# Optimization experiments

Measured on AMD Instinct MI355X. Metric: run time of the kernel, lower is better.

The kernel has to match this reference:

```python
import jax, jax.numpy as jnp
import numpy as np

N, E = 50000, 640000
IN, HD, OUT, NCLS = 768, 128, 128, 2
H, C = 4, 32  # heads, per-head channels (HD/H = OUT/H = 32)
NEG_SLOPE = 0.2


def _glorot(key, shape):
    fan_in, fan_out = shape[0], shape[1]
    lim = jnp.sqrt(6.0 / (fan_in + fan_out))
    return jax.random.uniform(key, shape, jnp.float32, -lim, lim)


def setup_inputs() -> dict:
    key = jax.random.key(0)
    ks = jax.random.split(key, 24)
    x = jax.random.normal(ks[0], (1, N, IN), jnp.float32)
    edge_index = jax.random.randint(ks[1], (2, E), 0, N, jnp.int64)
    d = {"x": x, "edge_index": edge_index}
    ins = [IN, HD, HD, HD]
    for i in range(4):
        d[f"Wl{i+1}"] = _glorot(ks[2 + 5 * i], (ins[i], H * C))
        d[f"Wr{i+1}"] = _glorot(ks[3 + 5 * i], (ins[i], H * C))
        d[f"att{i+1}"] = _glorot(ks[4 + 5 * i], (H, C))
        d[f"b{i+1}"] = jnp.zeros((H * C,), jnp.float32)
    d["clfW"] = _glorot(ks[22], (OUT, NCLS))
    d["clfb"] = jnp.zeros((NCLS,), jnp.float32)
    return d


def _gatv2_layer(x, Wl, Wr, att, b, src, dst):
    # x: [N, F_in] -> out: [N, H*C]. GATv2: e = a^T LeakyReLU(xl_j + xr_i)
    xl = (x @ Wl).reshape(N, H, C)
    xr = (x @ Wr).reshape(N, H, C)
    h = xl[src] + xr[dst]                                   # [E', H, C] per-edge gather
    e = jnp.einsum('ehc,hc->eh', jax.nn.leaky_relu(h, NEG_SLOPE), att)
    m = jax.ops.segment_max(e, dst, num_segments=N)          # scatter-softmax (stable)
    a = jnp.exp(e - m[dst])
    s = jax.ops.segment_sum(a, dst, num_segments=N)
    alpha = a / (s[dst] + 1e-16)
    out = jax.ops.segment_sum(alpha[..., None] * xl[src], dst, num_segments=N)
    return out.reshape(N, H * C) + b


def reference(x, edge_index, Wl1, Wr1, att1, b1, Wl2, Wr2, att2, b2,
              Wl3, Wr3, att3, b3, Wl4, Wr4, att4, b4, clfW, clfb):
    xn = x.reshape(N, IN)  # torch.squeeze
    loops = jnp.arange(N, dtype=edge_index.dtype)  # PyG add_self_loops=True
    src = jnp.concatenate([edge_index[0], loops])
    dst = jnp.concatenate([edge_index[1], loops])
    h = jax.nn.relu(_gatv2_layer(xn, Wl1, Wr1, att1, b1, src, dst))
    h = jax.nn.relu(_gatv2_layer(h, Wl2, Wr2, att2, b2, src, dst))
    h = jax.nn.relu(_gatv2_layer(h, Wl3, Wr3, att3, b3, src, dst))
    h = _gatv2_layer(h, Wl4, Wr4, att4, b4, src, dst)        # [N, OUT]
    g = jnp.mean(h, axis=0, keepdims=True)                   # unsqueeze+mean over nodes -> [1, OUT]
    return g @ clfW + clfb                                   # [1, NCLS]
```

## Files before the change

kernel.cpp:

```cpp
#include <hip/hip_runtime.h>
#include <hip/hip_bf16.h>
#include <hip/hip_fp16.h>

#define NN 50000
#define EE 640000
#define HC 128
#define NB1 196
#define NEB 6250

typedef _Float16 f16x8 __attribute__((ext_vector_type(8)));
typedef _Float16 h2 __attribute__((ext_vector_type(2)));
typedef float f32x4 __attribute__((ext_vector_type(4)));
typedef unsigned short u16;

__device__ __forceinline__ u16 f2h(float f) {
    return __builtin_bit_cast(u16, (_Float16)f);
}
__device__ __forceinline__ h2 bch2(unsigned a) { return __builtin_bit_cast(h2, a); }
__device__ __forceinline__ h2 habs2(h2 a) {
    return __builtin_bit_cast(h2, __builtin_bit_cast(unsigned, a) & 0x7FFF7FFFu);
}

__device__ __forceinline__ void gload_lds16(const void* g, void* l) {
    __builtin_amdgcn_global_load_lds((const __attribute__((address_space(1))) void*)g,
                                     (__attribute__((address_space(3))) void*)l, 16, 0, 0);
}

__device__ __forceinline__ float red8(float x) {
    x += __int_as_float(__builtin_amdgcn_update_dpp(0, __float_as_int(x), 0xB1, 0xF, 0xF, true));
    x += __int_as_float(__builtin_amdgcn_update_dpp(0, __float_as_int(x), 0x4E, 0xF, 0xF, true));
    x += __int_as_float(__builtin_amdgcn_ds_swizzle(__float_as_int(x), 0x101F));
    return x;
}


__global__ void k_count(const int* __restrict__ ei, int* __restrict__ cnt) {
    int e = blockIdx.x * blockDim.x + threadIdx.x;
    if (e < EE) atomicAdd(&cnt[ei[EE + e]], 1);
}

__global__ void k_bsum(const int* __restrict__ cnt, int* __restrict__ bsum) {
    __shared__ int sd[256];
    int b = blockIdx.x, t = threadIdx.x, i = b * 256 + t;
    sd[t] = (i < NN) ? cnt[i] + 1 : 0;
    __syncthreads();
    for (int o = 128; o; o >>= 1) { if (t < o) sd[t] += sd[t + o]; __syncthreads(); }
    if (!t) bsum[b] = sd[0];
}

__global__ void k_offs(const int* __restrict__ cnt_in, const int* __restrict__ bsum,
                       int* __restrict__ offs, int* __restrict__ cursor,
                       int* __restrict__ csr) {
    __shared__ int sb[256];
    __shared__ int sd[256];
    int b = blockIdx.x, t = threadIdx.x, i = b * 256 + t;
    sb[t] = (t < NB1) ? bsum[t] : 0;
    int v = (i < NN) ? cnt_in[i] + 1 : 0;
    sd[t] = v;
    __syncthreads();
    for (int o = 1; o < 256; o <<= 1) {
        int u1 = (t >= o) ? sd[t - o] : 0;
        int u2 = (t >= o) ? sb[t - o] : 0;
        __syncthreads();
        sd[t] += u1; sb[t] += u2;
        __syncthreads();
    }
    int bex = (b > 0) ? sb[b - 1] : 0;
    if (i < NN) {
        int o = bex + sd[t] - v;
        offs[i] = o;
        csr[o] = i;
        cursor[i] = o + 1;
    }
    if (b == NB1 - 1 && t == 0) offs[NN] = sb[NB1 - 1];
}

__global__ void k_fill(const int* __restrict__ ei, int* __restrict__ cursor,
                       int* __restrict__ csr) {
    int e = blockIdx.x * blockDim.x + threadIdx.x;
    if (e < EE) {
        int s = ei[e], d = ei[EE + e];
        int pos = atomicAdd(&cursor[d], 1);
        csr[pos] = s;
    }
}


#define WT_L0 196608
#define WT_LX 32768
#define WT_TOT (WT_L0 + 3 * WT_LX)

__global__ void k_castw_all(const float* __restrict__ Wl1, const float* __restrict__ Wr1,
                            const float* __restrict__ Wl2, const float* __restrict__ Wr2,
                            const float* __restrict__ Wl3, const float* __restrict__ Wr3,
                            const float* __restrict__ Wl4, const float* __restrict__ Wr4,
                            u16* __restrict__ WtAll) {
    int gid = blockIdx.x * 256 + threadIdx.x;
    if (gid >= WT_TOT) return;
    const float *Wl, *Wr;
    int idx, K, base;
    if (gid < WT_L0) { Wl = Wl1; Wr = Wr1; idx = gid; K = 768; base = 0; }
    else {
        int r = gid - WT_L0;
        int l = r >> 15; idx = r & (WT_LX - 1); K = 128; base = WT_L0 + l * WT_LX;
        if (l == 0)      { Wl = Wl2; Wr = Wr2; }
        else if (l == 1) { Wl = Wl3; Wr = Wr3; }
        else             { Wl = Wl4; Wr = Wr4; }
    }
    int c = idx / K, k = idx - c * K;
    float v = (c < 128) ? Wl[k * 128 + c] : Wr[k * 128 + (c - 128)];
    WtAll[base + idx] = f2h(v);
}


__global__ __launch_bounds__(512, 4)
void k_gemm0(const float* __restrict__ Af, const u16* __restrict__ Wt,
             u16* __restrict__ xb) {
    constexpr int K = 768;
    __shared__ __align__(16) u16 As[128 * 64];
    __shared__ __align__(16) u16 Bs[256 * 64];
    const int tid = threadIdx.x;
    const int wv = tid >> 6, ln = tid & 63;
    const int wr = wv >> 2, wc = wv & 3;
    const int m0 = blockIdx.x * 128;
    const int lrow = ln & 15, g = ln >> 4;

    f32x4 acc[4][4] = {};

    const int arow = tid >> 2, aq = tid & 3;
    int arg = m0 + arow; if (arg >= NN) arg = 0;
    float4 ra0, ra1, ra2, ra3;

    {
        const float* src = Af + (size_t)arg * K + aq * 16;
        ra0 = *(const float4*)(src);
        ra1 = *(const float4*)(src + 4);
        ra2 = *(const float4*)(src + 8);
        ra3 = *(const float4*)(src + 12);
    }

    constexpr int NSTEP = K / 64;
    for (int ks = 0; ks < NSTEP; ++ks) {
        {
            const int s = arow & 7;
            f16x8 v0, v1;
            v0[0] = (_Float16)ra0.x; v0[1] = (_Float16)ra0.y;
            v0[2] = (_Float16)ra0.z; v0[3] = (_Float16)ra0.w;
            v0[4] = (_Float16)ra1.x; v0[5] = (_Float16)ra1.y;
            v0[6] = (_Float16)ra1.z; v0[7] = (_Float16)ra1.w;
            v1[0] = (_Float16)ra2.x; v1[1] = (_Float16)ra2.y;
            v1[2] = (_Float16)ra2.z; v1[3] = (_Float16)ra2.w;
            v1[4] = (_Float16)ra3.x; v1[5] = (_Float16)ra3.y;
            v1[6] = (_Float16)ra3.z; v1[7] = (_Float16)ra3.w;
            *(f16x8*)&As[arow * 64 + (((aq * 2) ^ s) * 8)] = v0;
            *(f16x8*)&As[arow * 64 + (((aq * 2 + 1) ^ s) * 8)] = v1;
        }
        #pragma unroll
        for (int q = 0; q < 4; ++q) {
            int r8 = (wv * 4 + q) * 8;
            int row = r8 + (ln >> 3);
            int lc = (ln & 7) ^ (row & 7);
            gload_lds16(Wt + (size_t)row * K + ks * 64 + lc * 8, &Bs[r8 * 64]);
        }
        __syncthreads();

        if (ks + 1 < NSTEP) {
            const float* src = Af + (size_t)arg * K + (ks + 1) * 64 + aq * 16;
            ra0 = *(const float4*)(src);
            ra1 = *(const float4*)(src + 4);
            ra2 = *(const float4*)(src + 8);
            ra3 = *(const float4*)(src + 12);
        }

        #pragma unroll
        for (int kk = 0; kk < 2; ++kk) {
            f16x8 af[4], bfr[4];
            #pragma unroll
            for (int f = 0; f < 4; ++f) {
                int r = wr * 64 + f * 16 + lrow;
                af[f] = *(const f16x8*)&As[r * 64 + (((kk * 4 + g) ^ (r & 7)) * 8)];
                int c = wc * 64 + f * 16 + lrow;
                bfr[f] = *(const f16x8*)&Bs[c * 64 + (((kk * 4 + g) ^ (c & 7)) * 8)];
            }
            #pragma unroll
            for (int i = 0; i < 4; ++i)
                #pragma unroll
                for (int j = 0; j < 4; ++j)
                    acc[i][j] = __builtin_amdgcn_mfma_f32_16x16x32_f16(af[i], bfr[j], acc[i][j], 0, 0, 0);
        }
        __syncthreads();
    }

    const int crow0 = m0 + wr * 64 + (g << 2);
    const int ccol0 = wc * 64 + lrow;
    #pragma unroll
    for (int i = 0; i < 4; ++i)
        #pragma unroll
        for (int rr = 0; rr < 4; ++rr) {
            int row = crow0 + i * 16 + rr;
            if (row < NN) {
                #pragma unroll
                for (int j = 0; j < 4; ++j)
                    xb[(size_t)row * 256 + ccol0 + j * 16] = f2h(acc[i][j][rr]);
            }
        }
}


__global__ __launch_bounds__(512)
void k_gemm_s(const u16* __restrict__ A, const u16* __restrict__ Wt,
              u16* __restrict__ xb) {
    __shared__ __align__(16) u16 As[128 * 128];
    const int tid = threadIdx.x;
    const int wv = tid >> 6, ln = tid & 63;
    const int wr = wv >> 2, wc = wv & 3;
    const int m0 = blockIdx.x * 128;
    const int lrow = ln & 15, g = ln >> 4;

    #pragma unroll
    for (int q = 0; q < 4; ++q) {
        int seg = wv * 4 + q;
        int row = seg * 4 + g;
        int lc = lrow ^ (row & 15);
        int rg = m0 + row; if (rg >= NN) rg = 0;
        gload_lds16(A + (size_t)rg * 128 + lc * 8, &As[seg * 512]);
    }
    f16x8 bfr[4][4];
    #pragma unroll
    for (int j = 0; j < 4; ++j) {
        int col = wc * 64 + j * 16 + lrow;
        #pragma unroll
        for (int kk = 0; kk < 4; ++kk)
            bfr[j][kk] = *(const f16x8*)&Wt[(size_t)col * 128 + kk * 32 + g * 8];
    }
    __syncthreads();

    f32x4 acc[4][4] = {};
    #pragma unroll
    for (int kk = 0; kk < 4; ++kk) {
        f16x8 af[4];
        #pragma unroll
        for (int f = 0; f < 4; ++f) {
            int r = wr * 64 + f * 16 + lrow;
            int pc = (kk * 4 + g) ^ (r & 15);
            af[f] = *(const f16x8*)&As[r * 128 + pc * 8];
        }
        #pragma unroll
        for (int i = 0; i < 4; ++i)
            #pragma unroll
            for (int j = 0; j < 4; ++j)
                acc[i][j] = __builtin_amdgcn_mfma_f32_16x16x32_f16(af[i], bfr[j][kk], acc[i][j], 0, 0, 0);
    }

    const int crow0 = m0 + wr * 64 + (g << 2);
    const int ccol0 = wc * 64 + lrow;
    #pragma unroll
    for (int i = 0; i < 4; ++i)
        #pragma unroll
        for (int rr = 0; rr < 4; ++rr) {
            int row = crow0 + i * 16 + rr;
            if (row < NN) {
                #pragma unroll
                for (int j = 0; j < 4; ++j)
                    xb[(size_t)row * 256 + ccol0 + j * 16] = f2h(acc[i][j][rr]);
            }
        }
}


__global__ __launch_bounds__(256)
void k_edge(const u16* __restrict__ xb, const float* __restrict__ att,
            const float* __restrict__ bias, const int* __restrict__ offs,
            const int* __restrict__ csr, u16* __restrict__ outb,
            float* __restrict__ part, int relu) {
    __shared__ float ps[HC];
    const int wv = threadIdx.x >> 6;
    const int ln = threadIdx.x & 63;
    const int half = ln >> 5, lh = ln & 31;
    const int i = blockIdx.x * 8 + wv * 2 + half;
    const int c4 = lh * 4;

    if (part && threadIdx.x < HC) ps[threadIdx.x] = 0.f;

    uint2 xrw = *(const uint2*)&xb[(size_t)i * 256 + 128 + c4];
    const h2 xr01 = bch2(xrw.x), xr23 = bch2(xrw.y);
    float4 av = *(const float4*)&att[c4];
    const h2 at01 = {(_Float16)av.x, (_Float16)av.y};
    const h2 at23 = {(_Float16)av.z, (_Float16)av.w};
    const h2 C06 = {(_Float16)0.6f, (_Float16)0.6f};
    const h2 C04 = {(_Float16)0.4f, (_Float16)0.4f};

    int beg = offs[i];
    int deg = offs[i + 1] - beg;
    int degO = __shfl_xor(deg, 32);
    int degM = (deg > degO) ? deg : degO;

    float m0v = -3.0e38f, s0v = 0.f, a00 = 0.f, a01 = 0.f, a02 = 0.f, a03 = 0.f;
    float m1v = -3.0e38f, s1v = 0.f, a10 = 0.f, a11 = 0.f, a12 = 0.f, a13 = 0.f;
    float m2v = -3.0e38f, s2v = 0.f, a20 = 0.f, a21 = 0.f, a22 = 0.f, a23 = 0.f;
    float m3v = -3.0e38f, s3v = 0.f, a30 = 0.f, a31 = 0.f, a32 = 0.f, a33 = 0.f;

#define GATH(k, jj) uint2 w##k = *(const uint2*)&xb[(size_t)(jj) * 256 + c4];
#define UPD(k, M, S, A0, A1, A2, A3, ok) { \
    h2 v01 = bch2(w##k.x), v23 = bch2(w##k.y); \
    h2 u01 = v01 + xr01, u23 = v23 + xr23; \
    h2 l01 = u01 * C06 + habs2(u01) * C04; \
    h2 l23 = u23 * C06 + habs2(u23) * C04; \
    float e = __builtin_amdgcn_fdot2(l01, at01, \
              __builtin_amdgcn_fdot2(l23, at23, 0.f, false), false); \
    e = red8(e); \
    float d = e - M; \
    float tt = __expf(-fabsf(d)); \
    bool ng = (d <= 0.f) || (!(ok)); \
    float c = ng ? 1.f : tt; \
    float ww = (ok) ? (ng ? tt : 1.f) : 0.f; \
    M = ng ? M : e; \
    S = S * c + ww; \
    A0 = A0 * c + ww * (float)v01[0]; A1 = A1 * c + ww * (float)v01[1]; \
    A2 = A2 * c + ww * (float)v23[0]; A3 = A3 * c + ww * (float)v23[1]; }

    for (int base = 0; base < degM; base += 32) {
        int idxv = (base + lh < deg) ? csr[beg + base + lh] : i;
        int lim = degM - base; if (lim > 32) lim = 32;
        int myl = deg - base;
        for (int p = 0; p < lim; p += 4) {
            int j0 = __shfl(idxv, p + 0, 32);
            int j1 = __shfl(idxv, p + 1, 32);
            int j2 = __shfl(idxv, p + 2, 32);
            int j3 = __shfl(idxv, p + 3, 32);
            GATH(0, j0) GATH(1, j1) GATH(2, j2) GATH(3, j3)
            UPD(0, m0v, s0v, a00, a01, a02, a03, (p + 0 < myl))
            UPD(1, m1v, s1v, a10, a11, a12, a13, (p + 1 < myl))
            UPD(2, m2v, s2v, a20, a21, a22, a23, (p + 2 < myl))
            UPD(3, m3v, s3v, a30, a31, a32, a33, (p + 3 < myl))
        }
    }
#undef GATH
#undef UPD

    float mm = fmaxf(fmaxf(m0v, m1v), fmaxf(m2v, m3v));
    float c0 = __expf(m0v - mm), c1 = __expf(m1v - mm);
    float c2 = __expf(m2v - mm), c3 = __expf(m3v - mm);
    float s = s0v * c0 + s1v * c1 + s2v * c2 + s3v * c3 + 1e-16f;
    float inv = 1.f / s;
    float4 bv = *(const float4*)&bias[c4];
    float o0 = (a00 * c0 + a10 * c1 + a20 * c2 + a30 * c3) * inv + bv.x;
    float o1 = (a01 * c0 + a11 * c1 + a21 * c2 + a31 * c3) * inv + bv.y;
    float o2 = (a02 * c0 + a12 * c1 + a22 * c2 + a32 * c3) * inv + bv.z;
    float o3 = (a03 * c0 + a13 * c1 + a23 * c2 + a33 * c3) * inv + bv.w;
    if (relu) {
        o0 = fmaxf(o0, 0.f); o1 = fmaxf(o1, 0.f);
        o2 = fmaxf(o2, 0.f); o3 = fmaxf(o3, 0.f);
    }
    if (outb) {
        uint2 pk;
        pk.x = (unsigned)f2h(o0) | ((unsigned)f2h(o1) << 16);
        pk.y = (unsigned)f2h(o2) | ((unsigned)f2h(o3) << 16);
        *(uint2*)&outb[(size_t)i * HC + c4] = pk;
    }
    if (part) {
        __syncthreads();
        atomicAdd(&ps[c4 + 0], o0);
        atomicAdd(&ps[c4 + 1], o1);
        atomicAdd(&ps[c4 + 2], o2);
        atomicAdd(&ps[c4 + 3], o3);
        __syncthreads();
        if (threadIdx.x < HC)
            part[(size_t)blockIdx.x * HC + threadIdx.x] = ps[threadIdx.x];
    }
}


__global__ __launch_bounds__(256)
void k_colsum(const float* __restrict__ h, float* __restrict__ gsum, int nr) {
    __shared__ float4 sd[8][32];
    int t = threadIdx.x;
    int c4 = t & 31, rl = t >> 5;
    float sx = 0.f, sy = 0.f, sz = 0.f, sw = 0.f;
    for (int r = blockIdx.x * 8 + rl; r < nr; r += 8 * gridDim.x) {
        float4 v = *(const float4*)&h[(size_t)r * HC + c4 * 4];
        sx += v.x; sy += v.y; sz += v.z; sw += v.w;
    }
    sd[rl][c4] = make_float4(sx, sy, sz, sw);
    __syncthreads();
    if (rl == 0) {
        float4 a = sd[0][c4];
        #pragma unroll
        for (int q = 1; q < 8; ++q) {
            float4 b = sd[q][c4];
            a.x += b.x; a.y += b.y; a.z += b.z; a.w += b.w;
        }
        atomicAdd(&gsum[c4 * 4 + 0], a.x);
        atomicAdd(&gsum[c4 * 4 + 1], a.y);
        atomicAdd(&gsum[c4 * 4 + 2], a.z);
        atomicAdd(&gsum[c4 * 4 + 3], a.w);
    }
}

__global__ void k_clf(const float* __restrict__ gsum, const float* __restrict__ W,
                      const float* __restrict__ bcls, float* __restrict__ out) {
    __shared__ float v[HC];
    int t = threadIdx.x;
    v[t] = gsum[t] * (1.f / (float)NN);
    __syncthreads();
    if (t < 2) {
        float r = 0.f;
        for (int k = 0; k < HC; ++k) r += v[k] * W[k * 2 + t];
        out[t] = r + bcls[t];
    }
}


extern "C" void kernel_launch(void* const* d_in, const int* in_sizes, int n_in,
                              void* d_out, int out_size, void* d_ws, size_t ws_size,
                              hipStream_t stream) {
    const float* x = (const float*)d_in[0];
    const int* ei = (const int*)d_in[1];
    const float *Wl[4], *Wr[4], *att[4], *bia[4];
    for (int l = 0; l < 4; ++l) {
        Wl[l] = (const float*)d_in[2 + 4 * l];
        Wr[l] = (const float*)d_in[3 + 4 * l];
        att[l] = (const float*)d_in[4 + 4 * l];
        bia[l] = (const float*)d_in[5 + 4 * l];
    }
    const float* clfW = (const float*)d_in[18];
    const float* clfb = (const float*)d_in[19];
    float* outp = (float*)d_out;

    char* w = (char*)d_ws;
    size_t o = 0;
    auto alloc = [&](size_t bytes) {
        char* p = w + o;
        o = (o + bytes + 255) & ~(size_t)255;
        return p;
    };
    int* cnt    = (int*)alloc((size_t)NN * 4);
    float* gsum = (float*)alloc(HC * 4);
    size_t zspan = o;
    int* offs  = (int*)alloc((size_t)(NN + 1) * 4);
    int* csr   = (int*)alloc((size_t)(EE + NN) * 4);
    int* bsum  = (int*)alloc((size_t)NB1 * 4);
    u16* WtAll = (u16*)alloc((size_t)WT_TOT * 2);
    u16* xb    = (u16*)alloc((size_t)NN * 256 * 2);
    u16* hb0   = (u16*)alloc((size_t)NN * HC * 2);
    u16* hb1   = (u16*)alloc((size_t)NN * HC * 2);
    float* part = (float*)alloc((size_t)NEB * HC * 4);

    hipMemsetAsync(cnt, 0, zspan, stream);
    k_count<<<(EE + 255) / 256, 256, 0, stream>>>(ei, cnt);
    k_bsum<<<NB1, 256, 0, stream>>>(cnt, bsum);
    k_offs<<<NB1, 256, 0, stream>>>(cnt, bsum, offs, cnt, csr);
    k_fill<<<(EE + 255) / 256, 256, 0, stream>>>(ei, cnt, csr);
    k_castw_all<<<(WT_TOT + 255) / 256, 256, 0, stream>>>(
        Wl[0], Wr[0], Wl[1], Wr[1], Wl[2], Wr[2], Wl[3], Wr[3], WtAll);

    const int GB = (NN + 127) / 128;
    const u16* Wt_l[4] = {WtAll, WtAll + WT_L0, WtAll + WT_L0 + WT_LX,
                          WtAll + WT_L0 + 2 * WT_LX};
    const u16* hb_in = nullptr;
    u16* hbb[2] = {hb0, hb1};
    for (int l = 0; l < 4; ++l) {
        if (l == 0) k_gemm0<<<GB, 512, 0, stream>>>(x, Wt_l[0], xb);
        else        k_gemm_s<<<GB, 512, 0, stream>>>(hb_in, Wt_l[l], xb);
        u16* ob = (l < 3) ? hbb[l & 1] : nullptr;
        float* pp = (l == 3) ? part : nullptr;
        k_edge<<<NEB, 256, 0, stream>>>(xb, att[l], bia[l], offs, csr, ob, pp,
                                        (l < 3) ? 1 : 0);
        hb_in = ob;
    }

    k_colsum<<<64, 256, 0, stream>>>(part, gsum, NEB);
    k_clf<<<1, 128, 0, stream>>>(gsum, clfW, clfb, outp);
}
```

Measured before the change: 372.0 us.

## Double-buffer GEMM weight loads, replace final-layer block partials with full output

In the shared-weight GEMM, B fragments are now loaded one k-slice ahead instead of all sixteen up front, which cuts register pressure and overlaps global loads with MFMAs. The final edge layer no longer reduces through shared-memory atomics and two block barriers. It writes the full fp32 per-node output, and a wider colsum grid reduces it. The reduction helper also swaps a ds_swizzle for a DPP row-rotate. The trade is an extra ~25MB fp32 write and read in exchange for removing the atomics and barriers.

```diff
diff --git a/kernel.cpp b/kernel.cpp
--- a/kernel.cpp
+++ b/kernel.cpp
@@ -29,7 +29,7 @@
 __device__ __forceinline__ float red8(float x) {
     x += __int_as_float(__builtin_amdgcn_update_dpp(0, __float_as_int(x), 0xB1, 0xF, 0xF, true));
     x += __int_as_float(__builtin_amdgcn_update_dpp(0, __float_as_int(x), 0x4E, 0xF, 0xF, true));
-    x += __int_as_float(__builtin_amdgcn_ds_swizzle(__float_as_int(x), 0x101F));
+    x += __int_as_float(__builtin_amdgcn_update_dpp(0, __float_as_int(x), 0x141, 0xF, 0xF, true));
     return x;
 }
 
@@ -225,19 +225,23 @@
         int rg = m0 + row; if (rg >= NN) rg = 0;
         gload_lds16(A + (size_t)rg * 128 + lc * 8, &As[seg * 512]);
     }
-    f16x8 bfr[4][4];
-    #pragma unroll
-    for (int j = 0; j < 4; ++j) {
-        int col = wc * 64 + j * 16 + lrow;
-        #pragma unroll
-        for (int kk = 0; kk < 4; ++kk)
-            bfr[j][kk] = *(const f16x8*)&Wt[(size_t)col * 128 + kk * 32 + g * 8];
-    }
+    const int bcol = wc * 64 + lrow;
+    f16x8 b0_ = *(const f16x8*)&Wt[(size_t)(bcol     ) * 128 + g * 8];
+    f16x8 b1_ = *(const f16x8*)&Wt[(size_t)(bcol + 16) * 128 + g * 8];
+    f16x8 b2_ = *(const f16x8*)&Wt[(size_t)(bcol + 32) * 128 + g * 8];
+    f16x8 b3_ = *(const f16x8*)&Wt[(size_t)(bcol + 48) * 128 + g * 8];
     __syncthreads();
 
     f32x4 acc[4][4] = {};
     #pragma unroll
     for (int kk = 0; kk < 4; ++kk) {
+        f16x8 n0_, n1_, n2_, n3_;
+        if (kk < 3) {
+            n0_ = *(const f16x8*)&Wt[(size_t)(bcol     ) * 128 + (kk + 1) * 32 + g * 8];
+            n1_ = *(const f16x8*)&Wt[(size_t)(bcol + 16) * 128 + (kk + 1) * 32 + g * 8];
+            n2_ = *(const f16x8*)&Wt[(size_t)(bcol + 32) * 128 + (kk + 1) * 32 + g * 8];
+            n3_ = *(const f16x8*)&Wt[(size_t)(bcol + 48) * 128 + (kk + 1) * 32 + g * 8];
+        }
         f16x8 af[4];
         #pragma unroll
         for (int f = 0; f < 4; ++f) {
@@ -246,10 +250,13 @@
             af[f] = *(const f16x8*)&As[r * 128 + pc * 8];
         }
         #pragma unroll
-        for (int i = 0; i < 4; ++i)
-            #pragma unroll
-            for (int j = 0; j < 4; ++j)
-                acc[i][j] = __builtin_amdgcn_mfma_f32_16x16x32_f16(af[i], bfr[j][kk], acc[i][j], 0, 0, 0);
+        for (int i = 0; i < 4; ++i) {
+            acc[i][0] = __builtin_amdgcn_mfma_f32_16x16x32_f16(af[i], b0_, acc[i][0], 0, 0, 0);
+            acc[i][1] = __builtin_amdgcn_mfma_f32_16x16x32_f16(af[i], b1_, acc[i][1], 0, 0, 0);
+            acc[i][2] = __builtin_amdgcn_mfma_f32_16x16x32_f16(af[i], b2_, acc[i][2], 0, 0, 0);
+            acc[i][3] = __builtin_amdgcn_mfma_f32_16x16x32_f16(af[i], b3_, acc[i][3], 0, 0, 0);
+        }
+        if (kk < 3) { b0_ = n0_; b1_ = n1_; b2_ = n2_; b3_ = n3_; }
     }
 
     const int crow0 = m0 + wr * 64 + (g << 2);
@@ -272,15 +279,12 @@
 void k_edge(const u16* __restrict__ xb, const float* __restrict__ att,
             const float* __restrict__ bias, const int* __restrict__ offs,
             const int* __restrict__ csr, u16* __restrict__ outb,
-            float* __restrict__ part, int relu) {
-    __shared__ float ps[HC];
+            float* __restrict__ outf, int relu) {
     const int wv = threadIdx.x >> 6;
     const int ln = threadIdx.x & 63;
     const int half = ln >> 5, lh = ln & 31;
     const int i = blockIdx.x * 8 + wv * 2 + half;
     const int c4 = lh * 4;
-
-    if (part && threadIdx.x < HC) ps[threadIdx.x] = 0.f;
 
     uint2 xrw = *(const uint2*)&xb[(size_t)i * 256 + 128 + c4];
     const h2 xr01 = bch2(xrw.x), xr23 = bch2(xrw.y);
@@ -358,26 +362,19 @@
         pk.y = (unsigned)f2h(o2) | ((unsigned)f2h(o3) << 16);
         *(uint2*)&outb[(size_t)i * HC + c4] = pk;
     }
-    if (part) {
-        __syncthreads();
-        atomicAdd(&ps[c4 + 0], o0);
-        atomicAdd(&ps[c4 + 1], o1);
-        atomicAdd(&ps[c4 + 2], o2);
-        atomicAdd(&ps[c4 + 3], o3);
-        __syncthreads();
-        if (threadIdx.x < HC)
-            part[(size_t)blockIdx.x * HC + threadIdx.x] = ps[threadIdx.x];
+    if (outf) {
+        *(float4*)&outf[(size_t)i * HC + c4] = make_float4(o0, o1, o2, o3);
     }
 }
 
 
 __global__ __launch_bounds__(256)
-void k_colsum(const float* __restrict__ h, float* __restrict__ gsum, int nr) {
+void k_colsum(const float* __restrict__ h, float* __restrict__ gsum) {
     __shared__ float4 sd[8][32];
     int t = threadIdx.x;
     int c4 = t & 31, rl = t >> 5;
     float sx = 0.f, sy = 0.f, sz = 0.f, sw = 0.f;
-    for (int r = blockIdx.x * 8 + rl; r < nr; r += 8 * gridDim.x) {
+    for (int r = blockIdx.x * 8 + rl; r < NN; r += 8 * gridDim.x) {
         float4 v = *(const float4*)&h[(size_t)r * HC + c4 * 4];
         sx += v.x; sy += v.y; sz += v.z; sw += v.w;
     }
@@ -444,7 +441,7 @@
     u16* xb    = (u16*)alloc((size_t)NN * 256 * 2);
     u16* hb0   = (u16*)alloc((size_t)NN * HC * 2);
     u16* hb1   = (u16*)alloc((size_t)NN * HC * 2);
-    float* part = (float*)alloc((size_t)NEB * HC * 4);
+    float* hfin = (float*)alloc((size_t)NN * HC * 4);
 
     hipMemsetAsync(cnt, 0, zspan, stream);
     k_count<<<(EE + 255) / 256, 256, 0, stream>>>(ei, cnt);
@@ -463,12 +460,12 @@
         if (l == 0) k_gemm0<<<GB, 512, 0, stream>>>(x, Wt_l[0], xb);
         else        k_gemm_s<<<GB, 512, 0, stream>>>(hb_in, Wt_l[l], xb);
         u16* ob = (l < 3) ? hbb[l & 1] : nullptr;
-        float* pp = (l == 3) ? part : nullptr;
-        k_edge<<<NEB, 256, 0, stream>>>(xb, att[l], bia[l], offs, csr, ob, pp,
+        float* of = (l == 3) ? hfin : nullptr;
+        k_edge<<<NEB, 256, 0, stream>>>(xb, att[l], bia[l], offs, csr, ob, of,
                                         (l < 3) ? 1 : 0);
         hb_in = ob;
     }
 
-    k_colsum<<<64, 256, 0, stream>>>(part, gsum, NEB);
+    k_colsum<<<504, 256, 0, stream>>>(hfin, gsum);
     k_clf<<<1, 128, 0, stream>>>(gsum, clfW, clfb, outp);
 }
```

New measurement: 381.6 us. +2.6%, slower.
